# Performance work log

Hardware: AMD Instinct MI355X
Metric: run time of the kernel (lower is better)

## Reference

```python
import jax, jax.numpy as jnp
import numpy as np

# dims: batch, samples, agents, obs_dim, action_dim, hidden
B, S, N, D, A, H = 512, 64, 8, 64, 16, 256
IN_DIM = (D + A) * N  # 640


def mish(x):
    return x * jnp.tanh(jax.nn.softplus(x))


def setup_inputs() -> dict:
    key = jax.random.key(0)
    ks = jax.random.split(key, 9)
    u = lambda k, shape, fan_in: jax.random.uniform(
        k, shape, jnp.float32, -1.0 / np.sqrt(fan_in), 1.0 / np.sqrt(fan_in))
    return {
        "state": jax.random.normal(ks[0], (B, N, D), jnp.float32),
        "action": jax.random.normal(ks[1], (B, N, A), jnp.float32),
        "W1": u(ks[2], (IN_DIM, H), IN_DIM),
        "b1": u(ks[3], (H,), IN_DIM),
        "W2": u(ks[4], (H, H), H),
        "b2": u(ks[5], (H,), H),
        "W3": u(ks[6], (H, 1), H),
        "b3": u(ks[7], (1,), H),
        # random grand-coalition permutations of the N agents, per (batch, sample)
        "perm": jnp.argsort(jax.random.uniform(ks[8], (B, S, N)), axis=-1).astype(jnp.int32),
    }


def reference(state, action, W1, b1, W2, b2, W3, b3, perm):
    # subcoalition mask [B,S,N,N]: torch builds one-hot(perm) @ tril(ones),
    # i.e. mask[b,s,i,j] = 1 iff j <= perm[b,s,i]
    subcoal = (jnp.arange(N) <= perm[..., None]).astype(state.dtype)
    # gathered actions in coalition order [B,S,N,A]: act_g[b,s,j] = action[b, perm[b,s,j]]
    act_g = action[jnp.arange(B)[:, None, None], perm]
    # masked subcoalition actions [B,S,N,N,A] -> [B,S,N,N*A]
    act = (act_g[:, :, None, :, :] * subcoal[..., None]).reshape(B, S, N, N * A)
    # flattened global obs broadcast over (sample, agent) axes [B,S,N,N*D]
    obs = jnp.broadcast_to(state.reshape(B, 1, 1, N * D), (B, S, N, N * D))
    x = jnp.concatenate([obs, act], axis=-1)  # [B,S,N,IN_DIM]
    # per-agent loop in torch uses shared q1 weights -> single batched MLP
    h = mish(x @ W1 + b1)
    h = mish(h @ W2 + b2)
    q = h @ W3 + b3                   # [B,S,N,1]
    q1 = q.mean(axis=1).squeeze(-1)   # mean over samples -> [B,N]
    return (q1, q1)
```

## Files before the change

kernel.cpp:

```cpp
#include <hip/hip_runtime.h>
#include <hip/hip_bf16.h>

typedef unsigned short ushort_t;
typedef __attribute__((ext_vector_type(8))) short short8;
typedef __attribute__((ext_vector_type(4))) float floatx4;


__device__ __forceinline__ float mish_f(float x) {
    float e = __expf(x);
    float w = fmaf(e, e + 2.0f, 2.0f);
    return x - 2.0f * x * __builtin_amdgcn_rcpf(w);
}

__device__ __forceinline__ unsigned f2bf_u(float f) {
    unsigned int u = __float_as_uint(f);
    return (u + 0x7fffu + ((u >> 16) & 1u)) >> 16;
}

__global__ __launch_bounds__(256) void prep_kernel(
        const float* __restrict__ state,
        const float* __restrict__ action,
        const float* __restrict__ W1,
        const float* __restrict__ W2,
        float* __restrict__ obsW,
        ushort_t* __restrict__ actW,
        ushort_t* __restrict__ W2T) {
    int bid = blockIdx.x;
    int t = threadIdx.x;
    if (bid < 2048) {
        int b = bid >> 2;
        int kc = bid & 3;
        const float* stp = state + (size_t)b * 512 + kc * 128;
        const float* w1p = W1 + (size_t)(kc * 128) * 256 + t;
        float a0 = 0.f, a1 = 0.f, a2 = 0.f, a3 = 0.f;
#pragma unroll 8
        for (int f = 0; f < 128; f += 4) {
            a0 = fmaf(stp[f + 0], w1p[(f + 0) * 256], a0);
            a1 = fmaf(stp[f + 1], w1p[(f + 1) * 256], a1);
            a2 = fmaf(stp[f + 2], w1p[(f + 2) * 256], a2);
            a3 = fmaf(stp[f + 3], w1p[(f + 3) * 256], a3);
        }
        atomicAdd(&obsW[b * 256 + t], (a0 + a1) + (a2 + a3));
    } else if (bid < 6144) {
        int idx = bid - 2048;
        int b = idx >> 3;
        int j = idx & 7;
        const float* acp = action + (size_t)b * 128;
        const float* W1a = W1 + (size_t)(512 + j * 16) * 256;
        float acc[8];
#pragma unroll
        for (int n = 0; n < 8; ++n) acc[n] = 0.f;
#pragma unroll
        for (int a = 0; a < 16; ++a) {
            float w = W1a[a * 256 + t];
#pragma unroll
            for (int n = 0; n < 8; ++n)
                acc[n] = fmaf(acp[n * 16 + a], w, acc[n]);
        }
#pragma unroll
        for (int n = 0; n < 8; ++n)
            actW[(((size_t)b * 8 + n) * 8 + j) * 256 + t] = (ushort_t)f2bf_u(acc[n]);
    } else {
        int n = (bid - 6144) * 4 + (t >> 6);
        int klo = (t & 63);
        for (int kk = 0; kk < 4; ++kk) {
            int k = kk * 64 + klo;
            W2T[n * 256 + k] = (ushort_t)f2bf_u(W2[k * 256 + n]);
        }
    }
}

#define LDK 264

__global__ __launch_bounds__(256, 4) void main_kernel(
        const float* __restrict__ obsW, const ushort_t* __restrict__ actW,
        const ushort_t* __restrict__ W2T, const int* __restrict__ perm,
        const float* __restrict__ b1, const float* __restrict__ b2,
        const float* __restrict__ W3, const float* __restrict__ b3,
        float* __restrict__ qk) {
    __shared__ ushort_t h1[64 * LDK];
    __shared__ float obsb[256];
    __shared__ int perm_s[64];
    __shared__ float qpart[4][64];

    int t = threadIdx.x;
    int bid = blockIdx.x;
    int b = (bid & 7) * 64 + ((bid >> 3) & 63);
    int sg = bid >> 9;
    int s0 = sg * 8;

    obsb[t] = obsW[b * 256 + t] + b1[t];
    if (t < 64) perm_s[t] = perm[((size_t)b * 64 + s0) * 8 + t];
    __syncthreads();

    const ushort_t* actb = actW + (size_t)b * 64 * 256;
    {
        int half = t >> 7;
        int c = (t & 127) * 2;
        float ob0 = obsb[c], ob1 = obsb[c + 1];
#pragma unroll
        for (int sl2 = 0; sl2 < 4; ++sl2) {
            int sl = half * 4 + sl2;
            unsigned av[8];
#pragma unroll
            for (int j = 0; j < 8; ++j) {
                int p = perm_s[sl * 8 + j];
                av[j] = *reinterpret_cast<const unsigned*>(actb + (p * 8 + j) * 256 + c);
            }
            float r0 = ob0, r1 = ob1;
#pragma unroll
            for (int j = 0; j < 8; ++j) {
                r0 += __uint_as_float(av[j] << 16);
                r1 += __uint_as_float(av[j] & 0xffff0000u);
                __hip_bfloat162 pk = __float22bfloat162_rn(make_float2(mish_f(r0), mish_f(r1)));
                *reinterpret_cast<__hip_bfloat162*>(&h1[(sl * 8 + j) * LDK + c]) = pk;
            }
        }
    }
    __syncthreads();

    int w = t >> 6;
    int lo = t & 15;
    int q = (t >> 4) & 3;

    floatx4 acc[4][4];
#pragma unroll
    for (int mt = 0; mt < 4; ++mt)
#pragma unroll
        for (int nt = 0; nt < 4; ++nt)
            acc[mt][nt] = (floatx4){0.f, 0.f, 0.f, 0.f};

    const ushort_t* w2base = W2T + ((size_t)(w * 64 + lo)) * 256 + q * 8;

#pragma unroll
    for (int ks = 0; ks < 8; ++ks) {
        short8 afr[4];
#pragma unroll
        for (int mt = 0; mt < 4; ++mt)
            afr[mt] = *reinterpret_cast<const short8*>(&h1[(mt * 16 + lo) * LDK + ks * 32 + q * 8]);
        short8 bfr[4];
#pragma unroll
        for (int nt = 0; nt < 4; ++nt)
            bfr[nt] = *reinterpret_cast<const short8*>(w2base + nt * 16 * 256 + ks * 32);
#pragma unroll
        for (int mt = 0; mt < 4; ++mt)
#pragma unroll
            for (int nt = 0; nt < 4; ++nt)
                acc[mt][nt] = __builtin_amdgcn_mfma_f32_16x16x32_bf16(afr[mt], bfr[nt], acc[mt][nt], 0, 0, 0);
    }

    float b2c[4], w3c[4];
#pragma unroll
    for (int nt = 0; nt < 4; ++nt) {
        int col = w * 64 + nt * 16 + lo;
        b2c[nt] = b2[col];
        w3c[nt] = W3[col];
    }
#pragma unroll
    for (int mt = 0; mt < 4; ++mt) {
        float part[4] = {0.f, 0.f, 0.f, 0.f};
#pragma unroll
        for (int nt = 0; nt < 4; ++nt) {
#pragma unroll
            for (int r = 0; r < 4; ++r) {
                float h2 = mish_f(acc[mt][nt][r] + b2c[nt]);
                part[r] = fmaf(h2, w3c[nt], part[r]);
            }
        }
#pragma unroll
        for (int r = 0; r < 4; ++r) {
            float v = part[r];
            v += __shfl_xor(v, 1);
            v += __shfl_xor(v, 2);
            v += __shfl_xor(v, 4);
            v += __shfl_xor(v, 8);
            if (lo == 0) qpart[w][mt * 16 + q * 4 + r] = v;
        }
    }
    __syncthreads();
    if (t < 64) {
        float qv = qpart[0][t] + qpart[1][t] + qpart[2][t] + qpart[3][t] + b3[0];
        qk[((size_t)b * 64 + s0) * 8 + t] = qv;
    }
}

__global__ __launch_bounds__(256) void final_kernel(
        const float* __restrict__ qk,
        const int* __restrict__ perm,
        float* __restrict__ out) {
    __shared__ float qs[4][512];
    __shared__ int ps[4][512];
    int t = threadIdx.x;
    int w = t >> 6;
    int lane = t & 63;
    int b = blockIdx.x * 4 + w;
    for (int r = 0; r < 8; ++r) {
        qs[w][r * 64 + lane] = qk[(size_t)b * 512 + r * 64 + lane];
        ps[w][r * 64 + lane] = perm[(size_t)b * 512 + r * 64 + lane];
    }
    __syncthreads();
    int i = lane & 7;
    int s0 = lane >> 3;
    float v = 0.0f;
    for (int s = s0; s < 64; s += 8) v += qs[w][s * 8 + ps[w][s * 8 + i]];
    v += __shfl_xor(v, 8);
    v += __shfl_xor(v, 16);
    v += __shfl_xor(v, 32);
    if (lane < 8) {
        float r = v * (1.0f / 64.0f);
        out[b * 8 + i] = r;
        out[4096 + b * 8 + i] = r;
    }
}

extern "C" void kernel_launch(void* const* d_in, const int* in_sizes, int n_in,
                              void* d_out, int out_size, void* d_ws, size_t ws_size,
                              hipStream_t stream) {
    const float* state  = (const float*)d_in[0];
    const float* action = (const float*)d_in[1];
    const float* W1     = (const float*)d_in[2];
    const float* b1     = (const float*)d_in[3];
    const float* W2     = (const float*)d_in[4];
    const float* b2     = (const float*)d_in[5];
    const float* W3     = (const float*)d_in[6];
    const float* b3     = (const float*)d_in[7];
    const int*   perm   = (const int*)d_in[8];
    float* out = (float*)d_out;

    char* ws = (char*)d_ws;
    float*    obsW = (float*)ws;
    ushort_t* actW = (ushort_t*)(ws + 524288);
    ushort_t* W2T  = (ushort_t*)(ws + 524288 + 16777216);
    float*    qk   = (float*)(ws + 524288 + 16777216 + 131072);

    hipMemsetAsync(obsW, 0, 512 * 256 * sizeof(float), stream);
    prep_kernel<<<6208, 256, 0, stream>>>(state, action, W1, W2, obsW, actW, W2T);
    main_kernel<<<4096, 256, 0, stream>>>(obsW, actW, W2T, perm, b1, b2, W3, b3, qk);
    final_kernel<<<128, 256, 0, stream>>>(qk, perm, out);
}
```

Before: 184.8 us.

## Fuse final reduction into main kernel and widen main blocks to 512 threads

The obs projection no longer splits K into chunks with atomics; each block now does the full 512-long dot product and folds in b1. The main kernel runs 8 waves per block, each owning 32 output columns instead of 64, which halves per-thread accumulators and may raise occupancy. The separate final reduction kernel is removed: each block reduces its 8 samples per agent through perm and atomically adds into the zeroed output. This saves one launch and the qk round trip, at the cost of float atomics with nondeterministic summation order and more per-block syncs.

```diff
diff --git a/kernel.cpp b/kernel.cpp
--- a/kernel.cpp
+++ b/kernel.cpp
@@ -21,28 +21,28 @@
         const float* __restrict__ state,
         const float* __restrict__ action,
         const float* __restrict__ W1,
+        const float* __restrict__ b1,
         const float* __restrict__ W2,
         float* __restrict__ obsW,
         ushort_t* __restrict__ actW,
         ushort_t* __restrict__ W2T) {
     int bid = blockIdx.x;
     int t = threadIdx.x;
-    if (bid < 2048) {
-        int b = bid >> 2;
-        int kc = bid & 3;
-        const float* stp = state + (size_t)b * 512 + kc * 128;
-        const float* w1p = W1 + (size_t)(kc * 128) * 256 + t;
+    if (bid < 512) {
+        int b = bid;
+        const float* stp = state + (size_t)b * 512;
+        const float* w1p = W1 + t;
         float a0 = 0.f, a1 = 0.f, a2 = 0.f, a3 = 0.f;
 #pragma unroll 8
-        for (int f = 0; f < 128; f += 4) {
+        for (int f = 0; f < 512; f += 4) {
             a0 = fmaf(stp[f + 0], w1p[(f + 0) * 256], a0);
             a1 = fmaf(stp[f + 1], w1p[(f + 1) * 256], a1);
             a2 = fmaf(stp[f + 2], w1p[(f + 2) * 256], a2);
             a3 = fmaf(stp[f + 3], w1p[(f + 3) * 256], a3);
         }
-        atomicAdd(&obsW[b * 256 + t], (a0 + a1) + (a2 + a3));
-    } else if (bid < 6144) {
-        int idx = bid - 2048;
+        obsW[b * 256 + t] = (a0 + a1) + (a2 + a3) + b1[t];
+    } else if (bid < 4608) {
+        int idx = bid - 512;
         int b = idx >> 3;
         int j = idx & 7;
         const float* acp = action + (size_t)b * 128;
@@ -61,7 +61,7 @@
         for (int n = 0; n < 8; ++n)
             actW[(((size_t)b * 8 + n) * 8 + j) * 256 + t] = (ushort_t)f2bf_u(acc[n]);
     } else {
-        int n = (bid - 6144) * 4 + (t >> 6);
+        int n = (bid - 4608) * 4 + (t >> 6);
         int klo = (t & 63);
         for (int kk = 0; kk < 4; ++kk) {
             int k = kk * 64 + klo;
@@ -72,16 +72,17 @@
 
 #define LDK 264
 
-__global__ __launch_bounds__(256, 4) void main_kernel(
+__global__ __launch_bounds__(512, 8) void main_kernel(
         const float* __restrict__ obsW, const ushort_t* __restrict__ actW,
         const ushort_t* __restrict__ W2T, const int* __restrict__ perm,
-        const float* __restrict__ b1, const float* __restrict__ b2,
+        const float* __restrict__ b2,
         const float* __restrict__ W3, const float* __restrict__ b3,
-        float* __restrict__ qk) {
+        float* __restrict__ out) {
     __shared__ ushort_t h1[64 * LDK];
     __shared__ float obsb[256];
     __shared__ int perm_s[64];
-    __shared__ float qpart[4][64];
+    __shared__ float qpart[8][64];
+    __shared__ float qv_s[64];
 
     int t = threadIdx.x;
     int bid = blockIdx.x;
@@ -89,18 +90,18 @@
     int sg = bid >> 9;
     int s0 = sg * 8;
 
-    obsb[t] = obsW[b * 256 + t] + b1[t];
-    if (t < 64) perm_s[t] = perm[((size_t)b * 64 + s0) * 8 + t];
+    if (t < 256) obsb[t] = obsW[b * 256 + t];
+    else if (t < 320) perm_s[t - 256] = perm[((size_t)b * 64 + s0) * 8 + (t - 256)];
     __syncthreads();
 
     const ushort_t* actb = actW + (size_t)b * 64 * 256;
     {
-        int half = t >> 7;
+        int slg = t >> 7;
         int c = (t & 127) * 2;
         float ob0 = obsb[c], ob1 = obsb[c + 1];
 #pragma unroll
-        for (int sl2 = 0; sl2 < 4; ++sl2) {
-            int sl = half * 4 + sl2;
+        for (int sl2 = 0; sl2 < 2; ++sl2) {
+            int sl = slg * 2 + sl2;
             unsigned av[8];
 #pragma unroll
             for (int j = 0; j < 8; ++j) {
@@ -120,17 +121,18 @@
     __syncthreads();
 
     int w = t >> 6;
-    int lo = t & 15;
-    int q = (t >> 4) & 3;
-
-    floatx4 acc[4][4];
+    int L = t & 63;
+    int lo = L & 15;
+    int q = L >> 4;
+
+    floatx4 acc[4][2];
 #pragma unroll
     for (int mt = 0; mt < 4; ++mt)
 #pragma unroll
-        for (int nt = 0; nt < 4; ++nt)
+        for (int nt = 0; nt < 2; ++nt)
             acc[mt][nt] = (floatx4){0.f, 0.f, 0.f, 0.f};
 
-    const ushort_t* w2base = W2T + ((size_t)(w * 64 + lo)) * 256 + q * 8;
+    const ushort_t* w2base = W2T + ((size_t)(w * 32 + lo)) * 256 + q * 8;
 
 #pragma unroll
     for (int ks = 0; ks < 8; ++ks) {
@@ -138,21 +140,19 @@
 #pragma unroll
         for (int mt = 0; mt < 4; ++mt)
             afr[mt] = *reinterpret_cast<const short8*>(&h1[(mt * 16 + lo) * LDK + ks * 32 + q * 8]);
-        short8 bfr[4];
-#pragma unroll
-        for (int nt = 0; nt < 4; ++nt)
-            bfr[nt] = *reinterpret_cast<const short8*>(w2base + nt * 16 * 256 + ks * 32);
-#pragma unroll
-        for (int mt = 0; mt < 4; ++mt)
-#pragma unroll
-            for (int nt = 0; nt < 4; ++nt)
-                acc[mt][nt] = __builtin_amdgcn_mfma_f32_16x16x32_bf16(afr[mt], bfr[nt], acc[mt][nt], 0, 0, 0);
-    }
-
-    float b2c[4], w3c[4];
-#pragma unroll
-    for (int nt = 0; nt < 4; ++nt) {
-        int col = w * 64 + nt * 16 + lo;
+#pragma unroll
+        for (int nt = 0; nt < 2; ++nt) {
+            short8 bfr = *reinterpret_cast<const short8*>(w2base + nt * 16 * 256 + ks * 32);
+#pragma unroll
+            for (int mt = 0; mt < 4; ++mt)
+                acc[mt][nt] = __builtin_amdgcn_mfma_f32_16x16x32_bf16(afr[mt], bfr, acc[mt][nt], 0, 0, 0);
+        }
+    }
+
+    float b2c[2], w3c[2];
+#pragma unroll
+    for (int nt = 0; nt < 2; ++nt) {
+        int col = w * 32 + nt * 16 + lo;
         b2c[nt] = b2[col];
         w3c[nt] = W3[col];
     }
@@ -160,7 +160,7 @@
     for (int mt = 0; mt < 4; ++mt) {
         float part[4] = {0.f, 0.f, 0.f, 0.f};
 #pragma unroll
-        for (int nt = 0; nt < 4; ++nt) {
+        for (int nt = 0; nt < 2; ++nt) {
 #pragma unroll
             for (int r = 0; r < 4; ++r) {
                 float h2 = mish_f(acc[mt][nt][r] + b2c[nt]);
@@ -179,37 +179,20 @@
     }
     __syncthreads();
     if (t < 64) {
-        float qv = qpart[0][t] + qpart[1][t] + qpart[2][t] + qpart[3][t] + b3[0];
-        qk[((size_t)b * 64 + s0) * 8 + t] = qv;
-    }
-}
-
-__global__ __launch_bounds__(256) void final_kernel(
-        const float* __restrict__ qk,
-        const int* __restrict__ perm,
-        float* __restrict__ out) {
-    __shared__ float qs[4][512];
-    __shared__ int ps[4][512];
-    int t = threadIdx.x;
-    int w = t >> 6;
-    int lane = t & 63;
-    int b = blockIdx.x * 4 + w;
-    for (int r = 0; r < 8; ++r) {
-        qs[w][r * 64 + lane] = qk[(size_t)b * 512 + r * 64 + lane];
-        ps[w][r * 64 + lane] = perm[(size_t)b * 512 + r * 64 + lane];
-    }
-    __syncthreads();
-    int i = lane & 7;
-    int s0 = lane >> 3;
-    float v = 0.0f;
-    for (int s = s0; s < 64; s += 8) v += qs[w][s * 8 + ps[w][s * 8 + i]];
-    v += __shfl_xor(v, 8);
-    v += __shfl_xor(v, 16);
-    v += __shfl_xor(v, 32);
-    if (lane < 8) {
-        float r = v * (1.0f / 64.0f);
-        out[b * 8 + i] = r;
-        out[4096 + b * 8 + i] = r;
+        float qv = b3[0];
+#pragma unroll
+        for (int ww = 0; ww < 8; ++ww) qv += qpart[ww][t];
+        qv_s[t] = qv;
+    }
+    __syncthreads();
+    if (t < 8) {
+        float p = 0.f;
+#pragma unroll
+        for (int sl = 0; sl < 8; ++sl)
+            p += qv_s[sl * 8 + perm_s[sl * 8 + t]];
+        p *= (1.0f / 64.0f);
+        atomicAdd(&out[b * 8 + t], p);
+        atomicAdd(&out[4096 + b * 8 + t], p);
     }
 }
 
@@ -231,10 +214,8 @@
     float*    obsW = (float*)ws;
     ushort_t* actW = (ushort_t*)(ws + 524288);
     ushort_t* W2T  = (ushort_t*)(ws + 524288 + 16777216);
-    float*    qk   = (float*)(ws + 524288 + 16777216 + 131072);
-
-    hipMemsetAsync(obsW, 0, 512 * 256 * sizeof(float), stream);
-    prep_kernel<<<6208, 256, 0, stream>>>(state, action, W1, W2, obsW, actW, W2T);
-    main_kernel<<<4096, 256, 0, stream>>>(obsW, actW, W2T, perm, b1, b2, W3, b3, qk);
-    final_kernel<<<128, 256, 0, stream>>>(qk, perm, out);
-}
+
+    hipMemsetAsync(out, 0, (size_t)out_size * sizeof(float), stream);
+    prep_kernel<<<4672, 256, 0, stream>>>(state, action, W1, b1, W2, obsW, actW, W2T);
+    main_kernel<<<4096, 512, 0, stream>>>(obsW, actW, W2T, perm, b2, W3, b3, out);
+}
```

After: 181.8 us. Within noise of the previous version (-1.6%).
